# Performance work log

Measured on AMD Instinct MI355X. Metric: run time of the kernel, lower is better.

The kernel has to match this reference:

```python
import jax, jax.numpy as jnp
import numpy as np

B, S, D, H = 4, 2048, 1024, 16
HD = D // H


def setup_inputs() -> dict:
    key = jax.random.key(0)
    ks = jax.random.split(key, 12)
    sc = 1.0 / np.sqrt(D)
    inp = {
        'q': jax.random.normal(ks[0], (B, S, D), jnp.float32),
        'k': jax.random.normal(ks[1], (B, S, D), jnp.float32),
        'v': jax.random.normal(ks[2], (B, S, D), jnp.float32),
        # causal mask: 1 where masked (upper triangle), broadcasts over batch/heads
        'mask': jnp.triu(jnp.ones((S, S), jnp.float32), k=1),
        'Wq': jax.random.normal(ks[3], (D, D), jnp.float32) * sc,
        'bq': jax.random.normal(ks[4], (D,), jnp.float32) * sc,
        'Wk': jax.random.normal(ks[5], (D, D), jnp.float32) * sc,
        'bk': jax.random.normal(ks[6], (D,), jnp.float32) * sc,
        'Wv': jax.random.normal(ks[7], (D, D), jnp.float32) * sc,
        'bv': jax.random.normal(ks[8], (D,), jnp.float32) * sc,
        'Wo': jax.random.normal(ks[9], (D, D), jnp.float32) * sc,
        'bo': jax.random.normal(ks[10], (D,), jnp.float32) * sc,
    }
    return inp


def _split_heads(x):
    # [B,S,D] -> [B,H,S,HD]
    return x.reshape(B, S, H, HD).transpose(0, 2, 1, 3)


def reference(q, k, v, mask, Wq, bq, Wk, bk, Wv, bv, Wo, bo):
    qw = q @ Wq + bq
    kw = k @ Wk + bk
    vw = v @ Wv + bv
    qh, kh, vh = _split_heads(qw), _split_heads(kw), _split_heads(vw)
    scores = jnp.einsum('bhqd,bhkd->bhqk', qh, kh) / jnp.sqrt(jnp.float32(HD))
    scores = scores + mask * (-1e20)
    weights = jax.nn.softmax(scores, axis=-1)
    attn = jnp.einsum('bhqk,bhkd->bhqd', weights, vh)
    attn = attn.transpose(0, 2, 1, 3).reshape(B, S, D)
    return attn @ Wo + bo
```

## Files before the change

### kernel.cpp

```cpp
#include <hip/hip_runtime.h>
#include <hip/hip_bf16.h>
#include <stdint.h>

#define B_ 4
#define S_ 2048
#define D_ 1024
#define H_ 16
#define HD_ 64

typedef __bf16 bf16_t;
typedef __bf16 bf16x8 __attribute__((ext_vector_type(8)));
typedef __bf16 bf16x2_t __attribute__((ext_vector_type(2)));
typedef float f32x4 __attribute__((ext_vector_type(4)));
typedef int i32x4 __attribute__((ext_vector_type(4)));

#define MFMA(a, b, c) __builtin_amdgcn_mfma_f32_16x16x32_bf16((a), (b), (c), 0, 0, 0)
#define LOG2E 1.44269504088896340736f

__device__ __forceinline__ void gload_lds16(const void* g, void* l) {
  __builtin_amdgcn_global_load_lds(
      (const __attribute__((address_space(1))) uint32_t*)g,
      (__attribute__((address_space(3))) uint32_t*)l, 16, 0, 0);
}

__device__ __forceinline__ float max3f(float a, float b, float c) {
  float d;
  asm("v_max3_f32 %0, %1, %2, %3" : "=v"(d) : "v"(a), "v"(b), "v"(c));
  return d;
}

__global__ __launch_bounds__(256) void wt_kernel(const float* __restrict__ Wq,
                                                 const float* __restrict__ Wk,
                                                 const float* __restrict__ Wv,
                                                 const float* __restrict__ Wo,
                                                 bf16_t* __restrict__ wt0) {
  __shared__ float t[32][33];
  const int z = blockIdx.z;
  const float* w_ = z == 0 ? Wq : (z == 1 ? Wk : (z == 2 ? Wv : Wo));
  bf16_t* wt = wt0 + (size_t)z * (1u << 20);
  const int tx = threadIdx.x & 31, ty = threadIdx.x >> 5;
  const int n0 = blockIdx.x * 32, k0 = blockIdx.y * 32;
#pragma unroll
  for (int i = 0; i < 4; i++)
    t[ty + i * 8][tx] = w_[(size_t)(k0 + ty + i * 8) * D_ + n0 + tx];
  __syncthreads();
#pragma unroll
  for (int i = 0; i < 4; i++)
    wt[(size_t)(n0 + ty + i * 8) * D_ + k0 + tx] = (bf16_t)t[tx][ty + i * 8];
}

__global__ __launch_bounds__(256) void conv_kernel(const float* __restrict__ q,
                                                   const float* __restrict__ k,
                                                   const float* __restrict__ v,
                                                   bf16_t* __restrict__ out) {
  const int z = blockIdx.z;
  const float* src = z == 0 ? q : (z == 1 ? k : v);
  bf16_t* dst = out + (size_t)z * 8388608u;
  const size_t i = ((size_t)blockIdx.x * 256 + threadIdx.x) * 8;
  float4 x0 = *(const float4*)(src + i);
  float4 x1 = *(const float4*)(src + i + 4);
  bf16x8 vv;
  vv[0] = (bf16_t)x0.x; vv[1] = (bf16_t)x0.y; vv[2] = (bf16_t)x0.z; vv[3] = (bf16_t)x0.w;
  vv[4] = (bf16_t)x1.x; vv[5] = (bf16_t)x1.y; vv[6] = (bf16_t)x1.z; vv[7] = (bf16_t)x1.w;
  *(bf16x8*)(dst + i) = vv;
}

template <bool QKV>
__global__ __launch_bounds__(256) void mm_kernel(const bf16_t* __restrict__ A0,
                                                 const bf16_t* __restrict__ wt0,
                                                 const float* __restrict__ b0,
                                                 const float* __restrict__ b1,
                                                 const float* __restrict__ b2,
                                                 void* __restrict__ out0) {
  __shared__ bf16_t smem[32768];

  const int z = QKV ? blockIdx.z : 0;
  const bf16_t* A = A0 + (size_t)z * 8388608u;
  const bf16_t* WT = wt0 + (size_t)z * 1048576u;
  const float* bias = QKV ? (z == 0 ? b0 : (z == 1 ? b1 : b2)) : b0;

  const int tid = threadIdx.x;
  const int w = tid >> 6, l = tid & 63;
  const int lr = l & 15, lg = l >> 4;
  const int wm = w >> 1, wn = w & 1;
  const int ib = (int)blockIdx.y * 8 + (int)blockIdx.x;
  const int swz = (ib & 7) * 64 + (ib >> 3);
  const int m0 = (swz >> 3) * 128, n0 = (swz & 7) * 128;

  const int row0 = tid >> 3;
  const int ks = (tid & 7) ^ (row0 & 7);
  const bf16_t* aS = A + (size_t)(m0 + row0) * 1024 + ks * 8;
  const bf16_t* bS = WT + (size_t)(n0 + row0) * 1024 + ks * 8;
  const int wsl = w * 512;

  f32x4 acc[4][4];
#pragma unroll
  for (int mt = 0; mt < 4; mt++)
#pragma unroll
    for (int nt = 0; nt < 4; nt++) {
      f32x4 zz = {0.f, 0.f, 0.f, 0.f};
      acc[mt][nt] = zz;
    }

#define STAGE(bi, kt)                                                   \
  do {                                                                  \
    bf16_t* ad = smem + (bi) * 16384 + wsl;                             \
    bf16_t* bd = smem + (bi) * 16384 + 8192 + wsl;                      \
    _Pragma("unroll") for (int c = 0; c < 4; c++) {                     \
      gload_lds16(bS + (size_t)c * 32768 + (kt), bd + c * 2048);        \
      gload_lds16(aS + (size_t)c * 32768 + (kt), ad + c * 2048);        \
    }                                                                   \
  } while (0)

  STAGE(0, 0);
  STAGE(1, 64);
  asm volatile("s_waitcnt vmcnt(8)" ::: "memory");
  __builtin_amdgcn_s_barrier();
  __builtin_amdgcn_sched_barrier(0);

  int buf = 0;
  for (int jt = 0; jt < 16; ++jt) {
    const bf16_t* alds = smem + buf * 16384;
    const bf16_t* blds = alds + 8192;
#pragma unroll
    for (int kk = 0; kk < 2; kk++) {
      bf16x8 af[4], bfr[4];
#pragma unroll
      for (int mt = 0; mt < 4; mt++) {
        int row = wm * 64 + mt * 16 + lr;
        int kc = kk * 4 + lg;
        af[mt] = *reinterpret_cast<const bf16x8*>(alds + row * 64 + ((kc ^ (row & 7)) * 8));
      }
#pragma unroll
      for (int nt = 0; nt < 4; nt++) {
        int row = wn * 64 + nt * 16 + lr;
        int kc = kk * 4 + lg;
        bfr[nt] = *reinterpret_cast<const bf16x8*>(blds + row * 64 + ((kc ^ (row & 7)) * 8));
      }
#pragma unroll
      for (int mt = 0; mt < 4; mt++)
#pragma unroll
        for (int nt = 0; nt < 4; nt++)
          acc[mt][nt] = MFMA(af[mt], bfr[nt], acc[mt][nt]);
    }
    if (jt == 15) break;
    __builtin_amdgcn_sched_barrier(0);
    __builtin_amdgcn_s_barrier();
    __builtin_amdgcn_sched_barrier(0);
    const int tn = (jt + 2 < 16) ? jt + 2 : 15;
    STAGE(buf, tn * 64);
    asm volatile("s_waitcnt vmcnt(8)" ::: "memory");
    __builtin_amdgcn_s_barrier();
    __builtin_amdgcn_sched_barrier(0);
    buf ^= 1;
  }
#undef STAGE

  float bn[4];
#pragma unroll
  for (int nt = 0; nt < 4; nt++) bn[nt] = bias[n0 + wn * 64 + nt * 16 + lr];

  if (!QKV) {
    float* out = (float*)out0;
#pragma unroll
    for (int mt = 0; mt < 4; mt++)
#pragma unroll
      for (int nt = 0; nt < 4; nt++)
#pragma unroll
        for (int r = 0; r < 4; r++) {
          int m = m0 + wm * 64 + mt * 16 + lg * 4 + r;
          int n = n0 + wn * 64 + nt * 16 + lr;
          out[(size_t)m * D_ + n] = acc[mt][nt][r] + bn[nt];
        }
  } else if (z != 2) {
    bf16_t* out = (bf16_t*)out0 + (size_t)z * 8388608u;
    const float sc = z == 0 ? 0.125f : 1.0f;
#pragma unroll
    for (int mt = 0; mt < 4; mt++)
#pragma unroll
      for (int nt = 0; nt < 4; nt++)
#pragma unroll
        for (int r = 0; r < 4; r++) {
          int m = m0 + wm * 64 + mt * 16 + lg * 4 + r;
          int n = n0 + wn * 64 + nt * 16 + lr;
          float v = (acc[mt][nt][r] + bn[nt]) * sc;
          int b = m >> 11, s = m & 2047, h = n >> 6, hd = n & 63;
          out[(((size_t)(b * H_ + h) * S_ + s) << 6) + hd] = (bf16_t)v;
        }
  } else {
    bf16_t* out = (bf16_t*)out0 + (size_t)z * 8388608u;
    __syncthreads();
#pragma unroll
    for (int mt = 0; mt < 4; mt++)
#pragma unroll
      for (int nt = 0; nt < 4; nt++)
#pragma unroll
        for (int r = 0; r < 4; r++) {
          int ml = wm * 64 + mt * 16 + lg * 4 + r;
          int nl = wn * 64 + nt * 16 + lr;
          smem[nl * 136 + ml] = (bf16_t)(acc[mt][nt][r] + bn[nt]);
        }
    __syncthreads();
    const int b = m0 >> 11, sbase = m0 & 2047;
#pragma unroll
    for (int c = 0; c < 8; c++) {
      int ci = c * 256 + tid;
      int dl = ci >> 4, sc2 = ci & 15;
      int n = n0 + dl, h = n >> 6, hd = n & 63;
      bf16x8 v = *reinterpret_cast<const bf16x8*>(smem + dl * 136 + sc2 * 8);
      *reinterpret_cast<bf16x8*>(out + ((size_t)((b * H_ + h) << 6) + hd) * S_ + sbase + sc2 * 8) = v;
    }
  }
}

__global__ __launch_bounds__(256) void attn_k(const bf16_t* __restrict__ qh,
                                              const bf16_t* __restrict__ kh,
                                              const bf16_t* __restrict__ vt,
                                              bf16_t* __restrict__ attn) {
  __shared__ bf16_t kbuf[2][4096];
  __shared__ bf16_t vbuf[2][4096];

  const int tid = threadIdx.x, w = tid >> 6, l = tid & 63;
  const int lr = l & 15, lg = l >> 4;

  const int ib = (int)blockIdx.y * 16 + (int)blockIdx.x;
  const int xcd = ib & 7, slot = ib >> 3;
  const int bh = xcd * 8 + (slot & 7);
  const int pr = slot >> 3;
  const int b = bh >> 4, h = bh & 15;

  const int zr0 = tid >> 3, kc = tid & 7;
  const int sks = kc ^ (zr0 & 7);
  const int kprow0 = ((zr0 >> 5) & 1) * 32 + ((zr0 >> 2) & 3) * 8 + ((zr0 >> 4) & 1) * 4 + (zr0 & 3);
  const int zr1 = 32 + zr0;
  const int kprow1 = ((zr1 >> 5) & 1) * 32 + ((zr1 >> 2) & 3) * 8 + ((zr1 >> 4) & 1) * 4 + (zr1 & 3);
  const bf16_t* kbase0 = kh + ((size_t)bh * S_ + kprow0) * HD_ + sks * 8;
  const bf16_t* kbase1 = kh + ((size_t)bh * S_ + kprow1) * HD_ + sks * 8;
  const bf16_t* vbase0 = vt + ((size_t)bh * HD_ + zr0) * S_ + sks * 8;
  const bf16_t* vbase1 = vt + ((size_t)bh * HD_ + zr1) * S_ + sks * 8;

  const int xs7 = lr & 7;
  const int koffA = lr * 64 + ((lg ^ xs7) << 3);
  const int koffB = lr * 64 + (((lg ^ xs7) ^ 4) << 3);
  const int rowlim = w * 16 + lr;
  const int wsl = w * 512;

  bf16x8 ones;
#pragma unroll
  for (int i = 0; i < 8; i++) ones[i] = (bf16_t)1.0f;

  for (int half = 0; half < 2; half++) {
    const int qt = half ? (31 - pr) : pr;
    const int q0 = qt * 64 + w * 16;

    const bf16_t* qp = qh + ((size_t)bh * S_ + q0 + lr) * HD_ + lg * 8;
    bf16x8 qf0 = *(const bf16x8*)qp;
    bf16x8 qf1 = *(const bf16x8*)(qp + 32);

    float mi = -1e30f;
    f32x4 o[4], os;
#pragma unroll
    for (int nt = 0; nt < 4; nt++) {
      f32x4 z = {0.f, 0.f, 0.f, 0.f};
      o[nt] = z;
    }
    {
      f32x4 z = {0.f, 0.f, 0.f, 0.f};
      os = z;
    }

    const bf16_t *ks0 = kbase0, *ks1 = kbase1, *vs0 = vbase0, *vs1 = vbase1;
    int jsrc = 0;

#define ISSUE_STAGE(kd, vd)                                     \
    do {                                                        \
      gload_lds16(ks0, (kd));                                   \
      gload_lds16(ks1, (kd) + 2048);                            \
      gload_lds16(vs0, (vd));                                   \
      gload_lds16(vs1, (vd) + 2048);                            \
      if (jsrc < qt) {                                          \
        ks0 += 64 * HD_; ks1 += 64 * HD_; vs0 += 64; vs1 += 64; \
        jsrc++;                                                 \
      }                                                         \
    } while (0)

    asm volatile("s_waitcnt vmcnt(0)" ::: "memory");

    const bf16_t *rK = kbuf[0], *rV = vbuf[0];
    const bf16_t *rKn = kbuf[1], *rVn = vbuf[1];
    bf16_t *wK = &kbuf[1][wsl], *wV = &vbuf[1][wsl];
    bf16_t *wKn = &kbuf[0][wsl], *wVn = &vbuf[0][wsl];

    ISSUE_STAGE(wKn, wVn);

    for (int jt = 0; jt <= qt; jt++) {
      ISSUE_STAGE(wK, wV);
      asm volatile("s_waitcnt vmcnt(4)" ::: "memory");
      __builtin_amdgcn_s_barrier();
      __builtin_amdgcn_sched_barrier(0);

      f32x4 s[4];
      __builtin_amdgcn_s_setprio(1);
#pragma unroll
      for (int nt = 0; nt < 4; nt++) {
        bf16x8 kf0 = *(const bf16x8*)(rK + koffA + nt * 1024);
        bf16x8 kf1 = *(const bf16x8*)(rK + koffB + nt * 1024);
        f32x4 a = {0.f, 0.f, 0.f, 0.f};
        a = MFMA(kf0, qf0, a);
        a = MFMA(kf1, qf1, a);
        s[nt] = a;
      }
      __builtin_amdgcn_s_setprio(0);
      if (jt == qt) {
#pragma unroll
        for (int nt = 0; nt < 4; nt++) {
          int kvb = ((nt >> 1) << 5) + ((nt & 1) << 2) + lg * 8;
#pragma unroll
          for (int r = 0; r < 4; r++)
            if (kvb + r > rowlim) s[nt][r] = -1e30f;
        }
      }
      float m0 = max3f(s[0][0], s[0][1], s[0][2]);
      float m1 = max3f(s[0][3], s[1][0], s[1][1]);
      float m2 = max3f(s[1][2], s[1][3], s[2][0]);
      float m3 = max3f(s[2][1], s[2][2], s[2][3]);
      float m4 = max3f(s[3][0], s[3][1], s[3][2]);
      float mx = fmaxf(max3f(m0, m1, m2), max3f(m3, m4, s[3][3]));
      mx = fmaxf(mx, __shfl_xor(mx, 16));
      mx = fmaxf(mx, __shfl_xor(mx, 32));
      if (!__all(mx <= mi + 8.0f)) {
        float mn = fmaxf(mi, mx);
        float al = __builtin_amdgcn_exp2f((mi - mn) * LOG2E);
        mi = mn;
#pragma unroll
        for (int r = 0; r < 4; r++) {
          float alr = __shfl(al, lg * 4 + r);
          o[0][r] *= alr; o[1][r] *= alr; o[2][r] *= alr; o[3][r] *= alr;
          os[r] *= alr;
        }
      }
      const float msc = mi * LOG2E;
#pragma unroll
      for (int nt = 0; nt < 4; nt++)
#pragma unroll
        for (int r = 0; r < 4; r++)
          s[nt][r] = __builtin_amdgcn_exp2f(s[nt][r] * LOG2E - msc);
      uint32_t pk[8];
#pragma unroll
      for (int nt = 0; nt < 4; nt++) {
        bf16x2_t plo = {(bf16_t)s[nt][0], (bf16_t)s[nt][1]};
        bf16x2_t phi = {(bf16_t)s[nt][2], (bf16_t)s[nt][3]};
        pk[nt * 2] = __builtin_bit_cast(uint32_t, plo);
        pk[nt * 2 + 1] = __builtin_bit_cast(uint32_t, phi);
      }
      i32x4 w0 = {(int)pk[0], (int)pk[1], (int)pk[2], (int)pk[3]};
      i32x4 w1 = {(int)pk[4], (int)pk[5], (int)pk[6], (int)pk[7]};
      bf16x8 pa0 = __builtin_bit_cast(bf16x8, w0);
      bf16x8 pa1 = __builtin_bit_cast(bf16x8, w1);
      __builtin_amdgcn_s_setprio(1);
#pragma unroll
      for (int ntd = 0; ntd < 4; ntd++) {
        bf16x8 vf0 = *(const bf16x8*)(rV + koffA + ntd * 1024);
        bf16x8 vf1 = *(const bf16x8*)(rV + koffB + ntd * 1024);
        o[ntd] = MFMA(pa0, vf0, o[ntd]);
        o[ntd] = MFMA(pa1, vf1, o[ntd]);
      }
      os = MFMA(pa0, ones, os);
      os = MFMA(pa1, ones, os);
      __builtin_amdgcn_s_setprio(0);

      __builtin_amdgcn_sched_barrier(0);
      __builtin_amdgcn_s_barrier();
      __builtin_amdgcn_sched_barrier(0);
      { const bf16_t* t = rK; rK = rKn; rKn = t; t = rV; rV = rVn; rVn = t; }
      { bf16_t* t = wK; wK = wKn; wKn = t; t = wV; wV = wVn; wVn = t; }
    }
#undef ISSUE_STAGE
#pragma unroll
    for (int r = 0; r < 4; r++) {
      float rinv = 1.f / os[r];
      int srw = q0 + lg * 4 + r;
#pragma unroll
      for (int ntd = 0; ntd < 4; ntd++)
        attn[((size_t)(b * S_ + srw)) * D_ + h * 64 + ntd * 16 + lr] =
            (bf16_t)(o[ntd][r] * rinv);
    }
  }
}

extern "C" void kernel_launch(void* const* d_in, const int* in_sizes, int n_in,
                              void* d_out, int out_size, void* d_ws, size_t ws_size,
                              hipStream_t stream) {
  (void)in_sizes; (void)n_in; (void)out_size; (void)ws_size;
  const float* q  = (const float*)d_in[0];
  const float* k  = (const float*)d_in[1];
  const float* v  = (const float*)d_in[2];
  const float* Wq = (const float*)d_in[4];
  const float* bq = (const float*)d_in[5];
  const float* Wk = (const float*)d_in[6];
  const float* bk = (const float*)d_in[7];
  const float* Wv = (const float*)d_in[8];
  const float* bv = (const float*)d_in[9];
  const float* Wo = (const float*)d_in[10];
  const float* bo = (const float*)d_in[11];

  char* ws = (char*)d_ws;
  bf16_t* wt0  = (bf16_t*)(ws + (0ull << 20));
  bf16_t* wto  = (bf16_t*)(ws + (6ull << 20));
  bf16_t* qkvb = (bf16_t*)(ws + (8ull << 20));
  bf16_t* qhb  = (bf16_t*)(ws + (56ull << 20));
  bf16_t* khb  = (bf16_t*)(ws + (72ull << 20));
  bf16_t* vtb  = (bf16_t*)(ws + (88ull << 20));
  bf16_t* atb  = (bf16_t*)(ws + (8ull << 20));

  dim3 tb(256);
  wt_kernel<<<dim3(32, 32, 4), tb, 0, stream>>>(Wq, Wk, Wv, Wo, wt0);
  conv_kernel<<<dim3(4096, 1, 3), tb, 0, stream>>>(q, k, v, qkvb);
  mm_kernel<true><<<dim3(8, 64, 3), tb, 0, stream>>>(qkvb, wt0, bq, bk, bv, qhb);
  attn_k<<<dim3(16, 64), tb, 0, stream>>>(qhb, khb, vtb, atb);
  mm_kernel<false><<<dim3(8, 64), tb, 0, stream>>>(atb, wto, bo, nullptr, nullptr, d_out);
}
```

Before: 178.9 us.

## Fuse fp32-to-bf16 input conversion into QKV GEMM and enlarge attention query tiles

Removes the separate conversion kernel by having the QKV projection load fp32 activations into registers, convert them to bf16, and write them into LDS, while the weights still go through direct global-to-LDS loads. This avoids a full write and re-read of the bf16 copy of q, k and v. The attention kernel now gives each wave 32 query rows (128 per block) instead of 16. Each K/V tile staged in LDS is reused across twice as many queries, and waves skip fully masked tiles. The costs are more register pressure, a register-staged A path that may overlap less well with compute, and half as many attention blocks.

After: 171.1 us. 1.05x faster.

```diff
diff --git a/kernel.cpp b/kernel.cpp
--- a/kernel.cpp
+++ b/kernel.cpp
@@ -49,36 +49,190 @@
     wt[(size_t)(n0 + ty + i * 8) * D_ + k0 + tx] = (bf16_t)t[tx][ty + i * 8];
 }
 
-__global__ __launch_bounds__(256) void conv_kernel(const float* __restrict__ q,
-                                                   const float* __restrict__ k,
-                                                   const float* __restrict__ v,
-                                                   bf16_t* __restrict__ out) {
+__global__ __launch_bounds__(256) void qkv_mm(const float* __restrict__ Aq,
+                                              const float* __restrict__ Ak,
+                                              const float* __restrict__ Av,
+                                              const bf16_t* __restrict__ wt0,
+                                              const float* __restrict__ b0,
+                                              const float* __restrict__ b1,
+                                              const float* __restrict__ b2,
+                                              bf16_t* __restrict__ out0) {
+  __shared__ bf16_t smem[32768];
+
   const int z = blockIdx.z;
-  const float* src = z == 0 ? q : (z == 1 ? k : v);
-  bf16_t* dst = out + (size_t)z * 8388608u;
-  const size_t i = ((size_t)blockIdx.x * 256 + threadIdx.x) * 8;
-  float4 x0 = *(const float4*)(src + i);
-  float4 x1 = *(const float4*)(src + i + 4);
-  bf16x8 vv;
-  vv[0] = (bf16_t)x0.x; vv[1] = (bf16_t)x0.y; vv[2] = (bf16_t)x0.z; vv[3] = (bf16_t)x0.w;
-  vv[4] = (bf16_t)x1.x; vv[5] = (bf16_t)x1.y; vv[6] = (bf16_t)x1.z; vv[7] = (bf16_t)x1.w;
-  *(bf16x8*)(dst + i) = vv;
-}
-
-template <bool QKV>
-__global__ __launch_bounds__(256) void mm_kernel(const bf16_t* __restrict__ A0,
-                                                 const bf16_t* __restrict__ wt0,
-                                                 const float* __restrict__ b0,
-                                                 const float* __restrict__ b1,
-                                                 const float* __restrict__ b2,
-                                                 void* __restrict__ out0) {
+  const float* Af = z == 0 ? Aq : (z == 1 ? Ak : Av);
+  const bf16_t* WT = wt0 + (size_t)z * 1048576u;
+  const float* bias = z == 0 ? b0 : (z == 1 ? b1 : b2);
+  bf16_t* out = out0 + (size_t)z * 8388608u;
+
+  const int tid = threadIdx.x;
+  const int w = tid >> 6, l = tid & 63;
+  const int lr = l & 15, lg = l >> 4;
+  const int wm = w >> 1, wn = w & 1;
+  const int ib = (int)blockIdx.y * 8 + (int)blockIdx.x;
+  const int swz = (ib & 7) * 64 + (ib >> 3);
+  const int m0 = (swz >> 3) * 128, n0 = (swz & 7) * 128;
+
+  const int row0 = tid >> 3;
+  const int ks = (tid & 7) ^ (row0 & 7);
+  const float* aSf = Af + (size_t)(m0 + row0) * 1024 + ks * 8;
+  const bf16_t* bS = WT + (size_t)(n0 + row0) * 1024 + ks * 8;
+  const int wsl = w * 512;
+
+  f32x4 acc[4][4];
+#pragma unroll
+  for (int mt = 0; mt < 4; mt++)
+#pragma unroll
+    for (int nt = 0; nt < 4; nt++) {
+      f32x4 zz = {0.f, 0.f, 0.f, 0.f};
+      acc[mt][nt] = zz;
+    }
+
+  float4 aLoA[4], aHiA[4], aLoB[4], aHiB[4];
+
+#define STAGE_B(bi, kt)                                              \
+  do {                                                               \
+    bf16_t* bd = smem + (bi) * 16384 + 8192 + wsl;                   \
+    _Pragma("unroll") for (int c = 0; c < 4; c++)                    \
+        gload_lds16(bS + (size_t)c * 32768 + (kt), bd + c * 2048);   \
+  } while (0)
+
+#define LOADA(kt, Lo, Hi)                                            \
+  do {                                                               \
+    _Pragma("unroll") for (int c = 0; c < 4; c++) {                  \
+      Lo[c] = *(const float4*)(aSf + (size_t)c * 32768 + (kt));      \
+      Hi[c] = *(const float4*)(aSf + (size_t)c * 32768 + (kt) + 4);  \
+    }                                                                \
+  } while (0)
+
+#define WRITEA(bi, Lo, Hi)                                           \
+  do {                                                               \
+    _Pragma("unroll") for (int c = 0; c < 4; c++) {                  \
+      bf16x8 vv;                                                     \
+      vv[0] = (bf16_t)Lo[c].x; vv[1] = (bf16_t)Lo[c].y;              \
+      vv[2] = (bf16_t)Lo[c].z; vv[3] = (bf16_t)Lo[c].w;              \
+      vv[4] = (bf16_t)Hi[c].x; vv[5] = (bf16_t)Hi[c].y;              \
+      vv[6] = (bf16_t)Hi[c].z; vv[7] = (bf16_t)Hi[c].w;              \
+      *(bf16x8*)(smem + (bi) * 16384 + c * 2048 + tid * 8) = vv;     \
+    }                                                                \
+  } while (0)
+
+#define COMPUTE(bi)                                                              \
+  do {                                                                           \
+    const bf16_t* alds = smem + (bi) * 16384;                                    \
+    const bf16_t* blds = alds + 8192;                                            \
+    _Pragma("unroll") for (int kk = 0; kk < 2; kk++) {                           \
+      bf16x8 af[4], bfr[4];                                                      \
+      _Pragma("unroll") for (int mt = 0; mt < 4; mt++) {                         \
+        int row = wm * 64 + mt * 16 + lr;                                        \
+        int kc = kk * 4 + lg;                                                    \
+        af[mt] = *(const bf16x8*)(alds + row * 64 + ((kc ^ (row & 7)) * 8));     \
+      }                                                                          \
+      _Pragma("unroll") for (int nt = 0; nt < 4; nt++) {                         \
+        int row = wn * 64 + nt * 16 + lr;                                        \
+        int kc = kk * 4 + lg;                                                    \
+        bfr[nt] = *(const bf16x8*)(blds + row * 64 + ((kc ^ (row & 7)) * 8));    \
+      }                                                                          \
+      _Pragma("unroll") for (int mt = 0; mt < 4; mt++)                           \
+          _Pragma("unroll") for (int nt = 0; nt < 4; nt++)                       \
+              acc[mt][nt] = MFMA(af[mt], bfr[nt], acc[mt][nt]);                  \
+    }                                                                            \
+  } while (0)
+
+  STAGE_B(0, 0);
+  LOADA(0, aLoA, aHiA);
+  STAGE_B(1, 64);
+  LOADA(64, aLoB, aHiB);
+  asm volatile("s_waitcnt vmcnt(12)" ::: "memory");
+  WRITEA(0, aLoA, aHiA);
+  asm volatile("s_waitcnt lgkmcnt(0)" ::: "memory");
+  __builtin_amdgcn_s_barrier();
+  __builtin_amdgcn_sched_barrier(0);
+
+  for (int jt = 0; jt < 16; jt += 2) {
+    COMPUTE(0);
+    __builtin_amdgcn_sched_barrier(0);
+    __builtin_amdgcn_s_barrier();
+    __builtin_amdgcn_sched_barrier(0);
+    {
+      const int kt2 = (jt + 2 < 16 ? jt + 2 : 15) * 64;
+      STAGE_B(0, kt2);
+      LOADA(kt2, aLoA, aHiA);
+    }
+    asm volatile("s_waitcnt vmcnt(12)" ::: "memory");
+    WRITEA(1, aLoB, aHiB);
+    asm volatile("s_waitcnt lgkmcnt(0)" ::: "memory");
+    __builtin_amdgcn_s_barrier();
+    __builtin_amdgcn_sched_barrier(0);
+    COMPUTE(1);
+    if (jt == 14) break;
+    __builtin_amdgcn_sched_barrier(0);
+    __builtin_amdgcn_s_barrier();
+    __builtin_amdgcn_sched_barrier(0);
+    {
+      const int kt3 = (jt + 3) * 64;
+      STAGE_B(1, kt3);
+      LOADA(kt3, aLoB, aHiB);
+    }
+    asm volatile("s_waitcnt vmcnt(12)" ::: "memory");
+    WRITEA(0, aLoA, aHiA);
+    asm volatile("s_waitcnt lgkmcnt(0)" ::: "memory");
+    __builtin_amdgcn_s_barrier();
+    __builtin_amdgcn_sched_barrier(0);
+  }
+#undef STAGE_B
+#undef LOADA
+#undef WRITEA
+#undef COMPUTE
+
+  float bn[4];
+#pragma unroll
+  for (int nt = 0; nt < 4; nt++) bn[nt] = bias[n0 + wn * 64 + nt * 16 + lr];
+
+  if (z != 2) {
+    const float sc = z == 0 ? 0.125f : 1.0f;
+#pragma unroll
+    for (int mt = 0; mt < 4; mt++)
+#pragma unroll
+      for (int nt = 0; nt < 4; nt++)
+#pragma unroll
+        for (int r = 0; r < 4; r++) {
+          int m = m0 + wm * 64 + mt * 16 + lg * 4 + r;
+          int n = n0 + wn * 64 + nt * 16 + lr;
+          float v = (acc[mt][nt][r] + bn[nt]) * sc;
+          int b = m >> 11, s = m & 2047, h = n >> 6, hd = n & 63;
+          out[(((size_t)(b * H_ + h) * S_ + s) << 6) + hd] = (bf16_t)v;
+        }
+  } else {
+    __syncthreads();
+#pragma unroll
+    for (int mt = 0; mt < 4; mt++)
+#pragma unroll
+      for (int nt = 0; nt < 4; nt++)
+#pragma unroll
+        for (int r = 0; r < 4; r++) {
+          int ml = wm * 64 + mt * 16 + lg * 4 + r;
+          int nl = wn * 64 + nt * 16 + lr;
+          smem[nl * 136 + ml] = (bf16_t)(acc[mt][nt][r] + bn[nt]);
+        }
+    __syncthreads();
+    const int b = m0 >> 11, sbase = m0 & 2047;
+#pragma unroll
+    for (int c = 0; c < 8; c++) {
+      int ci = c * 256 + tid;
+      int dl = ci >> 4, sc2 = ci & 15;
+      int n = n0 + dl, h = n >> 6, hd = n & 63;
+      bf16x8 v = *reinterpret_cast<const bf16x8*>(smem + dl * 136 + sc2 * 8);
+      *reinterpret_cast<bf16x8*>(out + ((size_t)((b * H_ + h) << 6) + hd) * S_ + sbase + sc2 * 8) = v;
+    }
+  }
+}
+
+__global__ __launch_bounds__(256) void out_gemm(const bf16_t* __restrict__ A,
+                                                const bf16_t* __restrict__ WT,
+                                                const float* __restrict__ bias,
+                                                float* __restrict__ out) {
   __shared__ bf16_t smem[32768];
-
-  const int z = QKV ? blockIdx.z : 0;
-  const bf16_t* A = A0 + (size_t)z * 8388608u;
-  const bf16_t* WT = wt0 + (size_t)z * 1048576u;
-  const float* bias = QKV ? (z == 0 ? b0 : (z == 1 ? b1 : b2)) : b0;
-
   const int tid = threadIdx.x;
   const int w = tid >> 6, l = tid & 63;
   const int lr = l & 15, lg = l >> 4;
@@ -159,58 +313,16 @@
   float bn[4];
 #pragma unroll
   for (int nt = 0; nt < 4; nt++) bn[nt] = bias[n0 + wn * 64 + nt * 16 + lr];
-
-  if (!QKV) {
-    float* out = (float*)out0;
-#pragma unroll
-    for (int mt = 0; mt < 4; mt++)
-#pragma unroll
-      for (int nt = 0; nt < 4; nt++)
-#pragma unroll
-        for (int r = 0; r < 4; r++) {
-          int m = m0 + wm * 64 + mt * 16 + lg * 4 + r;
-          int n = n0 + wn * 64 + nt * 16 + lr;
-          out[(size_t)m * D_ + n] = acc[mt][nt][r] + bn[nt];
-        }
-  } else if (z != 2) {
-    bf16_t* out = (bf16_t*)out0 + (size_t)z * 8388608u;
-    const float sc = z == 0 ? 0.125f : 1.0f;
-#pragma unroll
-    for (int mt = 0; mt < 4; mt++)
-#pragma unroll
-      for (int nt = 0; nt < 4; nt++)
-#pragma unroll
-        for (int r = 0; r < 4; r++) {
-          int m = m0 + wm * 64 + mt * 16 + lg * 4 + r;
-          int n = n0 + wn * 64 + nt * 16 + lr;
-          float v = (acc[mt][nt][r] + bn[nt]) * sc;
-          int b = m >> 11, s = m & 2047, h = n >> 6, hd = n & 63;
-          out[(((size_t)(b * H_ + h) * S_ + s) << 6) + hd] = (bf16_t)v;
-        }
-  } else {
-    bf16_t* out = (bf16_t*)out0 + (size_t)z * 8388608u;
-    __syncthreads();
-#pragma unroll
-    for (int mt = 0; mt < 4; mt++)
-#pragma unroll
-      for (int nt = 0; nt < 4; nt++)
-#pragma unroll
-        for (int r = 0; r < 4; r++) {
-          int ml = wm * 64 + mt * 16 + lg * 4 + r;
-          int nl = wn * 64 + nt * 16 + lr;
-          smem[nl * 136 + ml] = (bf16_t)(acc[mt][nt][r] + bn[nt]);
-        }
-    __syncthreads();
-    const int b = m0 >> 11, sbase = m0 & 2047;
-#pragma unroll
-    for (int c = 0; c < 8; c++) {
-      int ci = c * 256 + tid;
-      int dl = ci >> 4, sc2 = ci & 15;
-      int n = n0 + dl, h = n >> 6, hd = n & 63;
-      bf16x8 v = *reinterpret_cast<const bf16x8*>(smem + dl * 136 + sc2 * 8);
-      *reinterpret_cast<bf16x8*>(out + ((size_t)((b * H_ + h) << 6) + hd) * S_ + sbase + sc2 * 8) = v;
-    }
-  }
+#pragma unroll
+  for (int mt = 0; mt < 4; mt++)
+#pragma unroll
+    for (int nt = 0; nt < 4; nt++)
+#pragma unroll
+      for (int r = 0; r < 4; r++) {
+        int m = m0 + wm * 64 + mt * 16 + lg * 4 + r;
+        int n = n0 + wn * 64 + nt * 16 + lr;
+        out[(size_t)m * D_ + n] = acc[mt][nt][r] + bn[nt];
+      }
 }
 
 __global__ __launch_bounds__(256) void attn_k(const bf16_t* __restrict__ qh,
@@ -223,7 +335,7 @@
   const int tid = threadIdx.x, w = tid >> 6, l = tid & 63;
   const int lr = l & 15, lg = l >> 4;
 
-  const int ib = (int)blockIdx.y * 16 + (int)blockIdx.x;
+  const int ib = (int)blockIdx.y * 8 + (int)blockIdx.x;
   const int xcd = ib & 7, slot = ib >> 3;
   const int bh = xcd * 8 + (slot & 7);
   const int pr = slot >> 3;
@@ -242,7 +354,9 @@
   const int xs7 = lr & 7;
   const int koffA = lr * 64 + ((lg ^ xs7) << 3);
   const int koffB = lr * 64 + (((lg ^ xs7) ^ 4) << 3);
-  const int rowlim = w * 16 + lr;
+  const int rowlim0 = w * 32 + lr;
+  const int rowlim1 = w * 32 + 16 + lr;
+  const int wact = w * 32 + 31;
   const int wsl = w * 512;
 
   bf16x8 ones;
@@ -250,23 +364,27 @@
   for (int i = 0; i < 8; i++) ones[i] = (bf16_t)1.0f;
 
   for (int half = 0; half < 2; half++) {
-    const int qt = half ? (31 - pr) : pr;
-    const int q0 = qt * 64 + w * 16;
-
-    const bf16_t* qp = qh + ((size_t)bh * S_ + q0 + lr) * HD_ + lg * 8;
-    bf16x8 qf0 = *(const bf16x8*)qp;
-    bf16x8 qf1 = *(const bf16x8*)(qp + 32);
-
-    float mi = -1e30f;
-    f32x4 o[4], os;
+    const int qt = half ? (15 - pr) : pr;
+    const int q0 = qt * 128 + w * 32;
+    const int jend = 2 * qt + 1;
+
+    const bf16_t* qp0 = qh + ((size_t)bh * S_ + q0 + lr) * HD_ + lg * 8;
+    const bf16_t* qp1 = qp0 + 16 * HD_;
+    bf16x8 qf00 = *(const bf16x8*)qp0;
+    bf16x8 qf01 = *(const bf16x8*)(qp0 + 32);
+    bf16x8 qf10 = *(const bf16x8*)qp1;
+    bf16x8 qf11 = *(const bf16x8*)(qp1 + 32);
+
+    float mi0 = -1e30f, mi1 = -1e30f;
+    f32x4 o0[4], o1[4], os0, os1;
 #pragma unroll
     for (int nt = 0; nt < 4; nt++) {
       f32x4 z = {0.f, 0.f, 0.f, 0.f};
-      o[nt] = z;
+      o0[nt] = z; o1[nt] = z;
     }
     {
       f32x4 z = {0.f, 0.f, 0.f, 0.f};
-      os = z;
+      os0 = z; os1 = z;
     }
 
     const bf16_t *ks0 = kbase0, *ks1 = kbase1, *vs0 = vbase0, *vs1 = vbase1;
@@ -278,7 +396,7 @@
       gload_lds16(ks1, (kd) + 2048);                            \
       gload_lds16(vs0, (vd));                                   \
       gload_lds16(vs1, (vd) + 2048);                            \
-      if (jsrc < qt) {                                          \
+      if (jsrc < jend) {                                        \
         ks0 += 64 * HD_; ks1 += 64 * HD_; vs0 += 64; vs1 += 64; \
         jsrc++;                                                 \
       }                                                         \
@@ -293,81 +411,116 @@
 
     ISSUE_STAGE(wKn, wVn);
 
-    for (int jt = 0; jt <= qt; jt++) {
+    for (int jt = 0; jt <= jend; jt++) {
       ISSUE_STAGE(wK, wV);
       asm volatile("s_waitcnt vmcnt(4)" ::: "memory");
       __builtin_amdgcn_s_barrier();
       __builtin_amdgcn_sched_barrier(0);
 
-      f32x4 s[4];
-      __builtin_amdgcn_s_setprio(1);
-#pragma unroll
-      for (int nt = 0; nt < 4; nt++) {
-        bf16x8 kf0 = *(const bf16x8*)(rK + koffA + nt * 1024);
-        bf16x8 kf1 = *(const bf16x8*)(rK + koffB + nt * 1024);
-        f32x4 a = {0.f, 0.f, 0.f, 0.f};
-        a = MFMA(kf0, qf0, a);
-        a = MFMA(kf1, qf1, a);
-        s[nt] = a;
+      const int doff = jt * 64 - qt * 128;
+      if (doff <= wact) {
+        f32x4 s0[4], s1[4];
+        __builtin_amdgcn_s_setprio(1);
+#pragma unroll
+        for (int nt = 0; nt < 4; nt++) {
+          bf16x8 kf0 = *(const bf16x8*)(rK + koffA + nt * 1024);
+          bf16x8 kf1 = *(const bf16x8*)(rK + koffB + nt * 1024);
+          f32x4 a = {0.f, 0.f, 0.f, 0.f};
+          a = MFMA(kf0, qf00, a);
+          a = MFMA(kf1, qf01, a);
+          s0[nt] = a;
+          f32x4 a2 = {0.f, 0.f, 0.f, 0.f};
+          a2 = MFMA(kf0, qf10, a2);
+          a2 = MFMA(kf1, qf11, a2);
+          s1[nt] = a2;
+        }
+        __builtin_amdgcn_s_setprio(0);
+        if (doff >= 0) {
+#pragma unroll
+          for (int nt = 0; nt < 4; nt++) {
+            int kvb = doff + ((nt >> 1) << 5) + ((nt & 1) << 2) + lg * 8;
+#pragma unroll
+            for (int r = 0; r < 4; r++) {
+              if (kvb + r > rowlim0) s0[nt][r] = -1e30f;
+              if (kvb + r > rowlim1) s1[nt][r] = -1e30f;
+            }
+          }
+        }
+        float ma0 = max3f(s0[0][0], s0[0][1], s0[0][2]);
+        float ma1 = max3f(s0[0][3], s0[1][0], s0[1][1]);
+        float ma2 = max3f(s0[1][2], s0[1][3], s0[2][0]);
+        float ma3 = max3f(s0[2][1], s0[2][2], s0[2][3]);
+        float ma4 = max3f(s0[3][0], s0[3][1], s0[3][2]);
+        float mx0 = fmaxf(max3f(ma0, ma1, ma2), max3f(ma3, ma4, s0[3][3]));
+        float mb0 = max3f(s1[0][0], s1[0][1], s1[0][2]);
+        float mb1 = max3f(s1[0][3], s1[1][0], s1[1][1]);
+        float mb2 = max3f(s1[1][2], s1[1][3], s1[2][0]);
+        float mb3 = max3f(s1[2][1], s1[2][2], s1[2][3]);
+        float mb4 = max3f(s1[3][0], s1[3][1], s1[3][2]);
+        float mx1 = fmaxf(max3f(mb0, mb1, mb2), max3f(mb3, mb4, s1[3][3]));
+        mx0 = fmaxf(mx0, __shfl_xor(mx0, 16));
+        mx0 = fmaxf(mx0, __shfl_xor(mx0, 32));
+        mx1 = fmaxf(mx1, __shfl_xor(mx1, 16));
+        mx1 = fmaxf(mx1, __shfl_xor(mx1, 32));
+        if (!__all((mx0 <= mi0 + 8.0f) && (mx1 <= mi1 + 8.0f))) {
+          float mn0 = fmaxf(mi0, mx0), mn1 = fmaxf(mi1, mx1);
+          float al0 = __builtin_amdgcn_exp2f((mi0 - mn0) * LOG2E);
+          float al1 = __builtin_amdgcn_exp2f((mi1 - mn1) * LOG2E);
+          mi0 = mn0; mi1 = mn1;
+#pragma unroll
+          for (int r = 0; r < 4; r++) {
+            float a0r = __shfl(al0, lg * 4 + r);
+            o0[0][r] *= a0r; o0[1][r] *= a0r; o0[2][r] *= a0r; o0[3][r] *= a0r;
+            os0[r] *= a0r;
+            float a1r = __shfl(al1, lg * 4 + r);
+            o1[0][r] *= a1r; o1[1][r] *= a1r; o1[2][r] *= a1r; o1[3][r] *= a1r;
+            os1[r] *= a1r;
+          }
+        }
+        const float msc0 = mi0 * LOG2E, msc1 = mi1 * LOG2E;
+#pragma unroll
+        for (int nt = 0; nt < 4; nt++)
+#pragma unroll
+          for (int r = 0; r < 4; r++) {
+            s0[nt][r] = __builtin_amdgcn_exp2f(s0[nt][r] * LOG2E - msc0);
+            s1[nt][r] = __builtin_amdgcn_exp2f(s1[nt][r] * LOG2E - msc1);
+          }
+        uint32_t pk0[8], pk1[8];
+#pragma unroll
+        for (int nt = 0; nt < 4; nt++) {
+          bf16x2_t p0lo = {(bf16_t)s0[nt][0], (bf16_t)s0[nt][1]};
+          bf16x2_t p0hi = {(bf16_t)s0[nt][2], (bf16_t)s0[nt][3]};
+          pk0[nt * 2] = __builtin_bit_cast(uint32_t, p0lo);
+          pk0[nt * 2 + 1] = __builtin_bit_cast(uint32_t, p0hi);
+          bf16x2_t p1lo = {(bf16_t)s1[nt][0], (bf16_t)s1[nt][1]};
+          bf16x2_t p1hi = {(bf16_t)s1[nt][2], (bf16_t)s1[nt][3]};
+          pk1[nt * 2] = __builtin_bit_cast(uint32_t, p1lo);
+          pk1[nt * 2 + 1] = __builtin_bit_cast(uint32_t, p1hi);
+        }
+        i32x4 w00 = {(int)pk0[0], (int)pk0[1], (int)pk0[2], (int)pk0[3]};
+        i32x4 w01 = {(int)pk0[4], (int)pk0[5], (int)pk0[6], (int)pk0[7]};
+        i32x4 w10 = {(int)pk1[0], (int)pk1[1], (int)pk1[2], (int)pk1[3]};
+        i32x4 w11 = {(int)pk1[4], (int)pk1[5], (int)pk1[6], (int)pk1[7]};
+        bf16x8 pa00 = __builtin_bit_cast(bf16x8, w00);
+        bf16x8 pa01 = __builtin_bit_cast(bf16x8, w01);
+        bf16x8 pa10 = __builtin_bit_cast(bf16x8, w10);
+        bf16x8 pa11 = __builtin_bit_cast(bf16x8, w11);
+        __builtin_amdgcn_s_setprio(1);
+#pragma unroll
+        for (int ntd = 0; ntd < 4; ntd++) {
+          bf16x8 vf0 = *(const bf16x8*)(rV + koffA + ntd * 1024);
+          bf16x8 vf1 = *(const bf16x8*)(rV + koffB + ntd * 1024);
+          o0[ntd] = MFMA(pa00, vf0, o0[ntd]);
+          o0[ntd] = MFMA(pa01, vf1, o0[ntd]);
+          o1[ntd] = MFMA(pa10, vf0, o1[ntd]);
+          o1[ntd] = MFMA(pa11, vf1, o1[ntd]);
+        }
+        os0 = MFMA(pa00, ones, os0);
+        os0 = MFMA(pa01, ones, os0);
+        os1 = MFMA(pa10, ones, os1);
+        os1 = MFMA(pa11, ones, os1);
+        __builtin_amdgcn_s_setprio(0);
       }
-      __builtin_amdgcn_s_setprio(0);
-      if (jt == qt) {
-#pragma unroll
-        for (int nt = 0; nt < 4; nt++) {
-          int kvb = ((nt >> 1) << 5) + ((nt & 1) << 2) + lg * 8;
-#pragma unroll
-          for (int r = 0; r < 4; r++)
-            if (kvb + r > rowlim) s[nt][r] = -1e30f;
-        }
-      }
-      float m0 = max3f(s[0][0], s[0][1], s[0][2]);
-      float m1 = max3f(s[0][3], s[1][0], s[1][1]);
-      float m2 = max3f(s[1][2], s[1][3], s[2][0]);
-      float m3 = max3f(s[2][1], s[2][2], s[2][3]);
-      float m4 = max3f(s[3][0], s[3][1], s[3][2]);
-      float mx = fmaxf(max3f(m0, m1, m2), max3f(m3, m4, s[3][3]));
-      mx = fmaxf(mx, __shfl_xor(mx, 16));
-      mx = fmaxf(mx, __shfl_xor(mx, 32));
-      if (!__all(mx <= mi + 8.0f)) {
-        float mn = fmaxf(mi, mx);
-        float al = __builtin_amdgcn_exp2f((mi - mn) * LOG2E);
-        mi = mn;
-#pragma unroll
-        for (int r = 0; r < 4; r++) {
-          float alr = __shfl(al, lg * 4 + r);
-          o[0][r] *= alr; o[1][r] *= alr; o[2][r] *= alr; o[3][r] *= alr;
-          os[r] *= alr;
-        }
-      }
-      const float msc = mi * LOG2E;
-#pragma unroll
-      for (int nt = 0; nt < 4; nt++)
-#pragma unroll
-        for (int r = 0; r < 4; r++)
-          s[nt][r] = __builtin_amdgcn_exp2f(s[nt][r] * LOG2E - msc);
-      uint32_t pk[8];
-#pragma unroll
-      for (int nt = 0; nt < 4; nt++) {
-        bf16x2_t plo = {(bf16_t)s[nt][0], (bf16_t)s[nt][1]};
-        bf16x2_t phi = {(bf16_t)s[nt][2], (bf16_t)s[nt][3]};
-        pk[nt * 2] = __builtin_bit_cast(uint32_t, plo);
-        pk[nt * 2 + 1] = __builtin_bit_cast(uint32_t, phi);
-      }
-      i32x4 w0 = {(int)pk[0], (int)pk[1], (int)pk[2], (int)pk[3]};
-      i32x4 w1 = {(int)pk[4], (int)pk[5], (int)pk[6], (int)pk[7]};
-      bf16x8 pa0 = __builtin_bit_cast(bf16x8, w0);
-      bf16x8 pa1 = __builtin_bit_cast(bf16x8, w1);
-      __builtin_amdgcn_s_setprio(1);
-#pragma unroll
-      for (int ntd = 0; ntd < 4; ntd++) {
-        bf16x8 vf0 = *(const bf16x8*)(rV + koffA + ntd * 1024);
-        bf16x8 vf1 = *(const bf16x8*)(rV + koffB + ntd * 1024);
-        o[ntd] = MFMA(pa0, vf0, o[ntd]);
-        o[ntd] = MFMA(pa1, vf1, o[ntd]);
-      }
-      os = MFMA(pa0, ones, os);
-      os = MFMA(pa1, ones, os);
-      __builtin_amdgcn_s_setprio(0);
 
       __builtin_amdgcn_sched_barrier(0);
       __builtin_amdgcn_s_barrier();
@@ -378,12 +531,17 @@
 #undef ISSUE_STAGE
 #pragma unroll
     for (int r = 0; r < 4; r++) {
-      float rinv = 1.f / os[r];
-      int srw = q0 + lg * 4 + r;
-#pragma unroll
-      for (int ntd = 0; ntd < 4; ntd++)
-        attn[((size_t)(b * S_ + srw)) * D_ + h * 64 + ntd * 16 + lr] =
-            (bf16_t)(o[ntd][r] * rinv);
+      float rinv0 = 1.f / os0[r];
+      float rinv1 = 1.f / os1[r];
+      int srw0 = q0 + lg * 4 + r;
+      int srw1 = srw0 + 16;
+#pragma unroll
+      for (int ntd = 0; ntd < 4; ntd++) {
+        attn[((size_t)(b * S_ + srw0)) * D_ + h * 64 + ntd * 16 + lr] =
+            (bf16_t)(o0[ntd][r] * rinv0);
+        attn[((size_t)(b * S_ + srw1)) * D_ + h * 64 + ntd * 16 + lr] =
+            (bf16_t)(o1[ntd][r] * rinv1);
+      }
     }
   }
 }
@@ -405,18 +563,16 @@
   const float* bo = (const float*)d_in[11];
 
   char* ws = (char*)d_ws;
-  bf16_t* wt0  = (bf16_t*)(ws + (0ull << 20));
-  bf16_t* wto  = (bf16_t*)(ws + (6ull << 20));
-  bf16_t* qkvb = (bf16_t*)(ws + (8ull << 20));
-  bf16_t* qhb  = (bf16_t*)(ws + (56ull << 20));
-  bf16_t* khb  = (bf16_t*)(ws + (72ull << 20));
-  bf16_t* vtb  = (bf16_t*)(ws + (88ull << 20));
-  bf16_t* atb  = (bf16_t*)(ws + (8ull << 20));
+  bf16_t* wt0 = (bf16_t*)(ws + (0ull << 20));
+  bf16_t* wto = (bf16_t*)(ws + (6ull << 20));
+  bf16_t* atb = (bf16_t*)(ws + (8ull << 20));
+  bf16_t* qhb = (bf16_t*)(ws + (56ull << 20));
+  bf16_t* khb = (bf16_t*)(ws + (72ull << 20));
+  bf16_t* vtb = (bf16_t*)(ws + (88ull << 20));
 
   dim3 tb(256);
   wt_kernel<<<dim3(32, 32, 4), tb, 0, stream>>>(Wq, Wk, Wv, Wo, wt0);
-  conv_kernel<<<dim3(4096, 1, 3), tb, 0, stream>>>(q, k, v, qkvb);
-  mm_kernel<true><<<dim3(8, 64, 3), tb, 0, stream>>>(qkvb, wt0, bq, bk, bv, qhb);
-  attn_k<<<dim3(16, 64), tb, 0, stream>>>(qhb, khb, vtb, atb);
-  mm_kernel<false><<<dim3(8, 64), tb, 0, stream>>>(atb, wto, bo, nullptr, nullptr, d_out);
-}
+  qkv_mm<<<dim3(8, 64, 3), tb, 0, stream>>>(q, k, v, wt0, bq, bk, bv, qhb);
+  attn_k<<<dim3(8, 64), tb, 0, stream>>>(qhb, khb, vtb, atb);
+  out_gemm<<<dim3(8, 64), tb, 0, stream>>>(atb, wto, bo, (float*)d_out);
+}
```

## Enlarge attention query tile to 128 rows with two 16-row sub-tiles per wave

Applied to the files above, without the earlier changes.

Each wave now processes 32 query rows (two 16-row MFMA tiles) instead of 16, so each block covers 128 queries and the grid halves. Each K/V tile loaded into LDS is reused across twice as many queries, which cuts LDS-load and global K/V traffic per unit of work. Waves skip fully masked KV tiles near the diagonal. The cost is more registers per thread, less occupancy, fewer blocks to balance causal work across CUs, and idle waves on diagonal tiles.

Measured after the change: 175.9 us. No clear change (-1.7%).

```diff
diff --git a/kernel.cpp b/kernel.cpp
--- a/kernel.cpp
+++ b/kernel.cpp
@@ -223,7 +223,7 @@
   const int tid = threadIdx.x, w = tid >> 6, l = tid & 63;
   const int lr = l & 15, lg = l >> 4;
 
-  const int ib = (int)blockIdx.y * 16 + (int)blockIdx.x;
+  const int ib = (int)blockIdx.y * 8 + (int)blockIdx.x;
   const int xcd = ib & 7, slot = ib >> 3;
   const int bh = xcd * 8 + (slot & 7);
   const int pr = slot >> 3;
@@ -242,7 +242,9 @@
   const int xs7 = lr & 7;
   const int koffA = lr * 64 + ((lg ^ xs7) << 3);
   const int koffB = lr * 64 + (((lg ^ xs7) ^ 4) << 3);
-  const int rowlim = w * 16 + lr;
+  const int rowlim0 = w * 32 + lr;
+  const int rowlim1 = w * 32 + 16 + lr;
+  const int wact = w * 32 + 31;
   const int wsl = w * 512;
 
   bf16x8 ones;
@@ -250,23 +252,27 @@
   for (int i = 0; i < 8; i++) ones[i] = (bf16_t)1.0f;
 
   for (int half = 0; half < 2; half++) {
-    const int qt = half ? (31 - pr) : pr;
-    const int q0 = qt * 64 + w * 16;
-
-    const bf16_t* qp = qh + ((size_t)bh * S_ + q0 + lr) * HD_ + lg * 8;
-    bf16x8 qf0 = *(const bf16x8*)qp;
-    bf16x8 qf1 = *(const bf16x8*)(qp + 32);
-
-    float mi = -1e30f;
-    f32x4 o[4], os;
+    const int qt = half ? (15 - pr) : pr;
+    const int q0 = qt * 128 + w * 32;
+    const int jend = 2 * qt + 1;
+
+    const bf16_t* qp0 = qh + ((size_t)bh * S_ + q0 + lr) * HD_ + lg * 8;
+    const bf16_t* qp1 = qp0 + 16 * HD_;
+    bf16x8 qf00 = *(const bf16x8*)qp0;
+    bf16x8 qf01 = *(const bf16x8*)(qp0 + 32);
+    bf16x8 qf10 = *(const bf16x8*)qp1;
+    bf16x8 qf11 = *(const bf16x8*)(qp1 + 32);
+
+    float mi0 = -1e30f, mi1 = -1e30f;
+    f32x4 o0[4], o1[4], os0, os1;
 #pragma unroll
     for (int nt = 0; nt < 4; nt++) {
       f32x4 z = {0.f, 0.f, 0.f, 0.f};
-      o[nt] = z;
+      o0[nt] = z; o1[nt] = z;
     }
     {
       f32x4 z = {0.f, 0.f, 0.f, 0.f};
-      os = z;
+      os0 = z; os1 = z;
     }
 
     const bf16_t *ks0 = kbase0, *ks1 = kbase1, *vs0 = vbase0, *vs1 = vbase1;
@@ -278,7 +284,7 @@
       gload_lds16(ks1, (kd) + 2048);                            \
       gload_lds16(vs0, (vd));                                   \
       gload_lds16(vs1, (vd) + 2048);                            \
-      if (jsrc < qt) {                                          \
+      if (jsrc < jend) {                                        \
         ks0 += 64 * HD_; ks1 += 64 * HD_; vs0 += 64; vs1 += 64; \
         jsrc++;                                                 \
       }                                                         \
@@ -293,81 +299,116 @@
 
     ISSUE_STAGE(wKn, wVn);
 
-    for (int jt = 0; jt <= qt; jt++) {
+    for (int jt = 0; jt <= jend; jt++) {
       ISSUE_STAGE(wK, wV);
       asm volatile("s_waitcnt vmcnt(4)" ::: "memory");
       __builtin_amdgcn_s_barrier();
       __builtin_amdgcn_sched_barrier(0);
 
-      f32x4 s[4];
-      __builtin_amdgcn_s_setprio(1);
-#pragma unroll
-      for (int nt = 0; nt < 4; nt++) {
-        bf16x8 kf0 = *(const bf16x8*)(rK + koffA + nt * 1024);
-        bf16x8 kf1 = *(const bf16x8*)(rK + koffB + nt * 1024);
-        f32x4 a = {0.f, 0.f, 0.f, 0.f};
-        a = MFMA(kf0, qf0, a);
-        a = MFMA(kf1, qf1, a);
-        s[nt] = a;
+      const int doff = jt * 64 - qt * 128;
+      if (doff <= wact) {
+        f32x4 s0[4], s1[4];
+        __builtin_amdgcn_s_setprio(1);
+#pragma unroll
+        for (int nt = 0; nt < 4; nt++) {
+          bf16x8 kf0 = *(const bf16x8*)(rK + koffA + nt * 1024);
+          bf16x8 kf1 = *(const bf16x8*)(rK + koffB + nt * 1024);
+          f32x4 a = {0.f, 0.f, 0.f, 0.f};
+          a = MFMA(kf0, qf00, a);
+          a = MFMA(kf1, qf01, a);
+          s0[nt] = a;
+          f32x4 a2 = {0.f, 0.f, 0.f, 0.f};
+          a2 = MFMA(kf0, qf10, a2);
+          a2 = MFMA(kf1, qf11, a2);
+          s1[nt] = a2;
+        }
+        __builtin_amdgcn_s_setprio(0);
+        if (doff >= 0) {
+#pragma unroll
+          for (int nt = 0; nt < 4; nt++) {
+            int kvb = doff + ((nt >> 1) << 5) + ((nt & 1) << 2) + lg * 8;
+#pragma unroll
+            for (int r = 0; r < 4; r++) {
+              if (kvb + r > rowlim0) s0[nt][r] = -1e30f;
+              if (kvb + r > rowlim1) s1[nt][r] = -1e30f;
+            }
+          }
+        }
+        float ma0 = max3f(s0[0][0], s0[0][1], s0[0][2]);
+        float ma1 = max3f(s0[0][3], s0[1][0], s0[1][1]);
+        float ma2 = max3f(s0[1][2], s0[1][3], s0[2][0]);
+        float ma3 = max3f(s0[2][1], s0[2][2], s0[2][3]);
+        float ma4 = max3f(s0[3][0], s0[3][1], s0[3][2]);
+        float mx0 = fmaxf(max3f(ma0, ma1, ma2), max3f(ma3, ma4, s0[3][3]));
+        float mb0 = max3f(s1[0][0], s1[0][1], s1[0][2]);
+        float mb1 = max3f(s1[0][3], s1[1][0], s1[1][1]);
+        float mb2 = max3f(s1[1][2], s1[1][3], s1[2][0]);
+        float mb3 = max3f(s1[2][1], s1[2][2], s1[2][3]);
+        float mb4 = max3f(s1[3][0], s1[3][1], s1[3][2]);
+        float mx1 = fmaxf(max3f(mb0, mb1, mb2), max3f(mb3, mb4, s1[3][3]));
+        mx0 = fmaxf(mx0, __shfl_xor(mx0, 16));
+        mx0 = fmaxf(mx0, __shfl_xor(mx0, 32));
+        mx1 = fmaxf(mx1, __shfl_xor(mx1, 16));
+        mx1 = fmaxf(mx1, __shfl_xor(mx1, 32));
+        if (!__all((mx0 <= mi0 + 8.0f) && (mx1 <= mi1 + 8.0f))) {
+          float mn0 = fmaxf(mi0, mx0), mn1 = fmaxf(mi1, mx1);
+          float al0 = __builtin_amdgcn_exp2f((mi0 - mn0) * LOG2E);
+          float al1 = __builtin_amdgcn_exp2f((mi1 - mn1) * LOG2E);
+          mi0 = mn0; mi1 = mn1;
+#pragma unroll
+          for (int r = 0; r < 4; r++) {
+            float a0r = __shfl(al0, lg * 4 + r);
+            o0[0][r] *= a0r; o0[1][r] *= a0r; o0[2][r] *= a0r; o0[3][r] *= a0r;
+            os0[r] *= a0r;
+            float a1r = __shfl(al1, lg * 4 + r);
+            o1[0][r] *= a1r; o1[1][r] *= a1r; o1[2][r] *= a1r; o1[3][r] *= a1r;
+            os1[r] *= a1r;
+          }
+        }
+        const float msc0 = mi0 * LOG2E, msc1 = mi1 * LOG2E;
+#pragma unroll
+        for (int nt = 0; nt < 4; nt++)
+#pragma unroll
+          for (int r = 0; r < 4; r++) {
+            s0[nt][r] = __builtin_amdgcn_exp2f(s0[nt][r] * LOG2E - msc0);
+            s1[nt][r] = __builtin_amdgcn_exp2f(s1[nt][r] * LOG2E - msc1);
+          }
+        uint32_t pk0[8], pk1[8];
+#pragma unroll
+        for (int nt = 0; nt < 4; nt++) {
+          bf16x2_t p0lo = {(bf16_t)s0[nt][0], (bf16_t)s0[nt][1]};
+          bf16x2_t p0hi = {(bf16_t)s0[nt][2], (bf16_t)s0[nt][3]};
+          pk0[nt * 2] = __builtin_bit_cast(uint32_t, p0lo);
+          pk0[nt * 2 + 1] = __builtin_bit_cast(uint32_t, p0hi);
+          bf16x2_t p1lo = {(bf16_t)s1[nt][0], (bf16_t)s1[nt][1]};
+          bf16x2_t p1hi = {(bf16_t)s1[nt][2], (bf16_t)s1[nt][3]};
+          pk1[nt * 2] = __builtin_bit_cast(uint32_t, p1lo);
+          pk1[nt * 2 + 1] = __builtin_bit_cast(uint32_t, p1hi);
+        }
+        i32x4 w00 = {(int)pk0[0], (int)pk0[1], (int)pk0[2], (int)pk0[3]};
+        i32x4 w01 = {(int)pk0[4], (int)pk0[5], (int)pk0[6], (int)pk0[7]};
+        i32x4 w10 = {(int)pk1[0], (int)pk1[1], (int)pk1[2], (int)pk1[3]};
+        i32x4 w11 = {(int)pk1[4], (int)pk1[5], (int)pk1[6], (int)pk1[7]};
+        bf16x8 pa00 = __builtin_bit_cast(bf16x8, w00);
+        bf16x8 pa01 = __builtin_bit_cast(bf16x8, w01);
+        bf16x8 pa10 = __builtin_bit_cast(bf16x8, w10);
+        bf16x8 pa11 = __builtin_bit_cast(bf16x8, w11);
+        __builtin_amdgcn_s_setprio(1);
+#pragma unroll
+        for (int ntd = 0; ntd < 4; ntd++) {
+          bf16x8 vf0 = *(const bf16x8*)(rV + koffA + ntd * 1024);
+          bf16x8 vf1 = *(const bf16x8*)(rV + koffB + ntd * 1024);
+          o0[ntd] = MFMA(pa00, vf0, o0[ntd]);
+          o0[ntd] = MFMA(pa01, vf1, o0[ntd]);
+          o1[ntd] = MFMA(pa10, vf0, o1[ntd]);
+          o1[ntd] = MFMA(pa11, vf1, o1[ntd]);
+        }
+        os0 = MFMA(pa00, ones, os0);
+        os0 = MFMA(pa01, ones, os0);
+        os1 = MFMA(pa10, ones, os1);
+        os1 = MFMA(pa11, ones, os1);
+        __builtin_amdgcn_s_setprio(0);
       }
-      __builtin_amdgcn_s_setprio(0);
-      if (jt == qt) {
-#pragma unroll
-        for (int nt = 0; nt < 4; nt++) {
-          int kvb = ((nt >> 1) << 5) + ((nt & 1) << 2) + lg * 8;
-#pragma unroll
-          for (int r = 0; r < 4; r++)
-            if (kvb + r > rowlim) s[nt][r] = -1e30f;
-        }
-      }
-      float m0 = max3f(s[0][0], s[0][1], s[0][2]);
-      float m1 = max3f(s[0][3], s[1][0], s[1][1]);
-      float m2 = max3f(s[1][2], s[1][3], s[2][0]);
-      float m3 = max3f(s[2][1], s[2][2], s[2][3]);
-      float m4 = max3f(s[3][0], s[3][1], s[3][2]);
-      float mx = fmaxf(max3f(m0, m1, m2), max3f(m3, m4, s[3][3]));
-      mx = fmaxf(mx, __shfl_xor(mx, 16));
-      mx = fmaxf(mx, __shfl_xor(mx, 32));
-      if (!__all(mx <= mi + 8.0f)) {
-        float mn = fmaxf(mi, mx);
-        float al = __builtin_amdgcn_exp2f((mi - mn) * LOG2E);
-        mi = mn;
-#pragma unroll
-        for (int r = 0; r < 4; r++) {
-          float alr = __shfl(al, lg * 4 + r);
-          o[0][r] *= alr; o[1][r] *= alr; o[2][r] *= alr; o[3][r] *= alr;
-          os[r] *= alr;
-        }
-      }
-      const float msc = mi * LOG2E;
-#pragma unroll
-      for (int nt = 0; nt < 4; nt++)
-#pragma unroll
-        for (int r = 0; r < 4; r++)
-          s[nt][r] = __builtin_amdgcn_exp2f(s[nt][r] * LOG2E - msc);
-      uint32_t pk[8];
-#pragma unroll
-      for (int nt = 0; nt < 4; nt++) {
-        bf16x2_t plo = {(bf16_t)s[nt][0], (bf16_t)s[nt][1]};
-        bf16x2_t phi = {(bf16_t)s[nt][2], (bf16_t)s[nt][3]};
-        pk[nt * 2] = __builtin_bit_cast(uint32_t, plo);
-        pk[nt * 2 + 1] = __builtin_bit_cast(uint32_t, phi);
-      }
-      i32x4 w0 = {(int)pk[0], (int)pk[1], (int)pk[2], (int)pk[3]};
-      i32x4 w1 = {(int)pk[4], (int)pk[5], (int)pk[6], (int)pk[7]};
-      bf16x8 pa0 = __builtin_bit_cast(bf16x8, w0);
-      bf16x8 pa1 = __builtin_bit_cast(bf16x8, w1);
-      __builtin_amdgcn_s_setprio(1);
-#pragma unroll
-      for (int ntd = 0; ntd < 4; ntd++) {
-        bf16x8 vf0 = *(const bf16x8*)(rV + koffA + ntd * 1024);
-        bf16x8 vf1 = *(const bf16x8*)(rV + koffB + ntd * 1024);
-        o[ntd] = MFMA(pa0, vf0, o[ntd]);
-        o[ntd] = MFMA(pa1, vf1, o[ntd]);
-      }
-      os = MFMA(pa0, ones, os);
-      os = MFMA(pa1, ones, os);
-      __builtin_amdgcn_s_setprio(0);
 
       __builtin_amdgcn_sched_barrier(0);
       __builtin_amdgcn_s_barrier();
@@ -378,12 +419,17 @@
 #undef ISSUE_STAGE
 #pragma unroll
     for (int r = 0; r < 4; r++) {
-      float rinv = 1.f / os[r];
-      int srw = q0 + lg * 4 + r;
-#pragma unroll
-      for (int ntd = 0; ntd < 4; ntd++)
-        attn[((size_t)(b * S_ + srw)) * D_ + h * 64 + ntd * 16 + lr] =
-            (bf16_t)(o[ntd][r] * rinv);
+      float rinv0 = 1.f / os0[r];
+      float rinv1 = 1.f / os1[r];
+      int srw0 = q0 + lg * 4 + r;
+      int srw1 = srw0 + 16;
+#pragma unroll
+      for (int ntd = 0; ntd < 4; ntd++) {
+        attn[((size_t)(b * S_ + srw0)) * D_ + h * 64 + ntd * 16 + lr] =
+            (bf16_t)(o0[ntd][r] * rinv0);
+        attn[((size_t)(b * S_ + srw1)) * D_ + h * 64 + ntd * 16 + lr] =
+            (bf16_t)(o1[ntd][r] * rinv1);
+      }
     }
   }
 }
@@ -417,6 +463,6 @@
   wt_kernel<<<dim3(32, 32, 4), tb, 0, stream>>>(Wq, Wk, Wv, Wo, wt0);
   conv_kernel<<<dim3(4096, 1, 3), tb, 0, stream>>>(q, k, v, qkvb);
   mm_kernel<true><<<dim3(8, 64, 3), tb, 0, stream>>>(qkvb, wt0, bq, bk, bv, qhb);
-  attn_k<<<dim3(16, 64), tb, 0, stream>>>(qhb, khb, vtb, atb);
+  attn_k<<<dim3(8, 64), tb, 0, stream>>>(qhb, khb, vtb, atb);
   mm_kernel<false><<<dim3(8, 64), tb, 0, stream>>>(atb, wto, bo, nullptr, nullptr, d_out);
 }
```
